# Kernel optimization log

Hardware: AMD Instinct MI355X
Metric: run time of the kernel (lower is better)

## Reference

```python
import jax, jax.numpy as jnp
import numpy as np

N = 100000

def gat_layer(x, src, dst, W, a_s, a_d, b, H, C, concat):
    # x: [N, F_in]; messages flow src -> dst, softmax grouped by dst (PyG GATConv)
    h = (x @ W).reshape(N, H, C)                       # [N,H,C]
    al_s = jnp.sum(h * a_s, axis=-1)                   # [N,H]
    al_d = jnp.sum(h * a_d, axis=-1)                   # [N,H]
    e = jax.nn.leaky_relu(al_s[src] + al_d[dst], 0.2)  # [E,H]
    m = jax.ops.segment_max(e, dst, num_segments=N)    # [N,H] per-dst max
    ex = jnp.exp(e - m[dst])
    s = jax.ops.segment_sum(ex, dst, num_segments=N)
    alpha = ex / (s[dst] + 1e-16)                      # [E,H]
    msg = h[src] * alpha[:, :, None]                   # [E,H,C]
    out = jax.ops.segment_sum(msg, dst, num_segments=N)  # [N,H,C]
    out = out.reshape(N, H * C) if concat else out.mean(axis=1)
    return out + b

def setup_inputs() -> dict:
    key = jax.random.key(0)
    ks = jax.random.split(key, 32)
    d = {}
    d['x'] = jax.random.normal(ks[0], (N, 128), dtype=jnp.float32)
    d['edge_index'] = jax.random.randint(ks[1], (2, 1600000), 0, N, dtype=jnp.int32)
    dims = [(128, 8, 8), (64, 8, 8), (64, 8, 8), (64, 8, 8), (64, 8, 40)]
    for i, (fin, H, C) in enumerate(dims, start=1):
        d[f'W{i}'] = jax.random.normal(ks[4 * i], (fin, H * C), dtype=jnp.float32) * 0.1
        d[f'as{i}'] = jax.random.normal(ks[4 * i + 1], (H, C), dtype=jnp.float32) * 0.1
        d[f'ad{i}'] = jax.random.normal(ks[4 * i + 2], (H, C), dtype=jnp.float32) * 0.1
        d[f'b{i}'] = jnp.zeros((H * C if i < 5 else C,), dtype=jnp.float32)
    return d

def reference(x, edge_index, W1, as1, ad1, b1, W2, as2, ad2, b2, W3, as3, ad3, b3, W4, as4, ad4, b4, W5, as5, ad5, b5):
    # add self-loops (PyG GATConv default add_self_loops=True)
    loop = jnp.arange(N, dtype=edge_index.dtype)
    src = jnp.concatenate([edge_index[0], loop])
    dst = jnp.concatenate([edge_index[1], loop])
    h = gat_layer(x, src, dst, W1, as1, ad1, b1, 8, 8, True)
    h = jax.nn.leaky_relu(h, 0.2)  # dropout is identity in eval mode
    h = gat_layer(h, src, dst, W2, as2, ad2, b2, 8, 8, True)
    h = jax.nn.leaky_relu(h, 0.2)
    h = gat_layer(h, src, dst, W3, as3, ad3, b3, 8, 8, True)
    h = jax.nn.leaky_relu(h, 0.2)
    h = gat_layer(h, src, dst, W4, as4, ad4, b4, 8, 8, True)
    h = jax.nn.leaky_relu(h, 0.2)
    h = gat_layer(h, src, dst, W5, as5, ad5, b5, 8, 40, False)
    return jax.nn.log_softmax(h, axis=1)
```

## Files before the change

kernel.cpp:

```cpp
#include <hip/hip_runtime.h>
#include <cstddef>
#include <cstdint>

static __device__ __forceinline__ float leaky(float x){ return x >= 0.f ? x : 0.2f*x; }
static __device__ __forceinline__ float bfl(unsigned short v){ return __uint_as_float(((unsigned)v)<<16); }
static __device__ __forceinline__ float blo(unsigned u){ return __uint_as_float(u<<16); }
static __device__ __forceinline__ float bhi(unsigned u){ return __uint_as_float(u & 0xffff0000u); }
static __device__ __forceinline__ unsigned bf16r(float f){
  unsigned u = __float_as_uint(f);
  return (u + 0x7fffu + ((u>>16)&1u)) >> 16;
}
static __device__ __forceinline__ unsigned pk(float lo, float hi){
  return bf16r(lo) | (bf16r(hi)<<16);
}

__global__ __launch_bounds__(256) void rs_hist1(const int* __restrict__ edst, int E, int N,
                                                int* __restrict__ hist, int NBLK, int Etot){
  __shared__ int lh[512];
  int t = threadIdx.x, b = blockIdx.x;
  lh[t] = 0; lh[t+256] = 0;
  __syncthreads();
  int base = b*8192;
  for (int i = 0; i < 32; i++){
    int e = base + t + i*256;
    if (e < Etot){
      int d = (e < E) ? edst[e] : (e - E);
      atomicAdd(&lh[d>>8], 1);
    }
  }
  __syncthreads();
  hist[(size_t)t*NBLK + b] = lh[t];
  hist[(size_t)(t+256)*NBLK + b] = lh[t+256];
}
__global__ __launch_bounds__(256) void s_bsum(const int* __restrict__ a, int* __restrict__ bsum, int L){
  __shared__ int sm[256];
  int t = threadIdx.x; int i = blockIdx.x*256 + t;
  sm[t] = (i < L) ? a[i] : 0;
  __syncthreads();
  #pragma unroll
  for (int o=128;o;o>>=1){ if (t<o) sm[t]+=sm[t+o]; __syncthreads(); }
  if (t==0) bsum[blockIdx.x] = sm[0];
}
__global__ __launch_bounds__(512) void k_bscan(const int* __restrict__ bsum, int* __restrict__ boff, int NB){
  __shared__ int sm[512];
  int t = threadIdx.x;
  int v = (t < NB) ? bsum[t] : 0;
  sm[t] = v; __syncthreads();
  for (int o=1;o<512;o<<=1){
    int u = (t>=o) ? sm[t-o] : 0;
    __syncthreads();
    sm[t] += u;
    __syncthreads();
  }
  if (t < NB) boff[t] = sm[t] - v;
  if (t == NB-1) boff[NB] = sm[t];
}
__global__ __launch_bounds__(256) void s_apply(const int* __restrict__ a, const int* __restrict__ boff,
                                               int* __restrict__ out, int L){
  __shared__ int sm[256];
  int t = threadIdx.x, b = blockIdx.x;
  int i = b*256 + t;
  int v = (i < L) ? a[i] : 0;
  sm[t] = v; __syncthreads();
  for (int o=1;o<256;o<<=1){
    int u = (t>=o) ? sm[t-o] : 0;
    __syncthreads();
    sm[t] += u;
    __syncthreads();
  }
  if (i < L) out[i] = boff[b] + sm[t] - v;
}
__global__ __launch_bounds__(256) void rs_scatter1(const int* __restrict__ esrc, const int* __restrict__ edst,
                                                   int E, int N, const int* __restrict__ hist2, int NBLK,
                                                   int* __restrict__ bufA, int Etot){
  __shared__ int gb[512];
  __shared__ int lcnt[512];
  int t = threadIdx.x, b = blockIdx.x;
  gb[t]     = hist2[(size_t)t*NBLK + b];
  gb[t+256] = hist2[(size_t)(t+256)*NBLK + b];
  lcnt[t] = 0; lcnt[t+256] = 0;
  __syncthreads();
  int base = b*8192;
  for (int i = 0; i < 32; i++){
    int e = base + t + i*256;
    if (e < Etot){
      int s, d;
      if (e < E){ s = esrc[e]; d = edst[e]; }
      else { s = e - E; d = s; }
      int bin = d >> 8;
      int r = atomicAdd(&lcnt[bin], 1);
      bufA[gb[bin] + r] = s | ((d & 255) << 17);
    }
  }
}
__global__ __launch_bounds__(256) void rs_lvl2(const int* __restrict__ bufA, const int* __restrict__ hist2,
                                               int NBLK, int* __restrict__ srcs, int* __restrict__ off,
                                               int N, int Etot){
  __shared__ int cnt[256];
  __shared__ int basev[256];
  int t = threadIdx.x, g = blockIdx.x;
  int beg = hist2[(size_t)g*NBLK];
  int end = (g < 511) ? hist2[(size_t)(g+1)*NBLK] : Etot;
  cnt[t] = 0;
  __syncthreads();
  for (int j = beg + t; j < end; j += 256)
    atomicAdd(&cnt[(bufA[j] >> 17) & 255], 1);
  __syncthreads();
  int v = cnt[t];
  for (int o=1;o<256;o<<=1){
    int u = (t>=o) ? cnt[t-o] : 0;
    __syncthreads();
    cnt[t] += u;
    __syncthreads();
  }
  basev[t] = cnt[t] - v;
  __syncthreads();
  cnt[t] = 0;
  __syncthreads();
  for (int j = beg + t; j < end; j += 256){
    int u = bufA[j];
    int lb = (u >> 17) & 255;
    int r = atomicAdd(&cnt[lb], 1);
    srcs[beg + basev[lb] + r] = u & 0x1FFFF;
  }
  int node = g*256 + t;
  if (node < N) off[node] = beg + basev[t];
  if (g == 0 && t == 0) off[N] = Etot;
}

template<int K, int M, bool IB, bool OB, bool AL>
__global__ __launch_bounds__(256) void k_gemm(
    const void* __restrict__ Ain, const float* __restrict__ W, int ldw, int col0,
    void* __restrict__ out, int N,
    const float* __restrict__ a_s, const float* __restrict__ a_d,
    unsigned short* __restrict__ alsO, float* __restrict__ aldO)
{
  constexpr int KT = 64;
  constexpr int TX = M/4;
  __shared__ alignas(16) float As[64][68];
  __shared__ alignas(16) float Ws[KT][M];
  __shared__ float asl[64], adl[64];
  int t = threadIdx.x;
  int base = blockIdx.x*64;
  int tx = t % TX, ty = t / TX;
  bool act = ty < 16;
  int n0 = ty*4, m0 = tx*4;
  if (AL && t < 64){ asl[t] = a_s[t]; adl[t] = a_d[t]; }
  float acc[4][4] = {};
  for (int kt=0; kt<K; kt+=KT){
    if (IB){
      const unsigned short* A16 = (const unsigned short*)Ain;
      for (int i=t; i<64*8; i+=256){
        int n = i >> 3, kq = i & 7;
        uint4 q = make_uint4(0,0,0,0);
        int gn = base + n;
        if (gn < N) q = *(const uint4*)(A16 + (size_t)gn*K + kt + kq*8);
        float* ap = &As[n][kq*8];
        ap[0]=blo(q.x); ap[1]=bhi(q.x); ap[2]=blo(q.y); ap[3]=bhi(q.y);
        ap[4]=blo(q.z); ap[5]=bhi(q.z); ap[6]=blo(q.w); ap[7]=bhi(q.w);
      }
    } else {
      const float* A = (const float*)Ain;
      for (int i=t; i<64*16; i+=256){
        int n  = i >> 4;
        int kq = i & 15;
        float4 v = make_float4(0.f,0.f,0.f,0.f);
        int gn = base + n;
        if (gn < N) v = *(const float4*)(A + (size_t)gn*K + kt + kq*4);
        As[n][kq*4+0]=v.x; As[n][kq*4+1]=v.y; As[n][kq*4+2]=v.z; As[n][kq*4+3]=v.w;
      }
    }
    for (int i=t; i<KT*(M/4); i+=256){
      int k = i/(M/4), mq = i%(M/4);
      *(float4*)&Ws[k][mq*4] = *(const float4*)(W + (size_t)(kt+k)*ldw + col0 + mq*4);
    }
    __syncthreads();
    if (act){
      #pragma unroll 4
      for (int k=0;k<KT;k+=4){
        float4 a0 = *(const float4*)&As[n0+0][k];
        float4 a1 = *(const float4*)&As[n0+1][k];
        float4 a2 = *(const float4*)&As[n0+2][k];
        float4 a3 = *(const float4*)&As[n0+3][k];
        float4 w0 = *(const float4*)&Ws[k+0][m0];
        float4 w1 = *(const float4*)&Ws[k+1][m0];
        float4 w2 = *(const float4*)&Ws[k+2][m0];
        float4 w3 = *(const float4*)&Ws[k+3][m0];
        acc[0][0]=fmaf(a0.x,w0.x,acc[0][0]); acc[0][1]=fmaf(a0.x,w0.y,acc[0][1]);
        acc[0][2]=fmaf(a0.x,w0.z,acc[0][2]); acc[0][3]=fmaf(a0.x,w0.w,acc[0][3]);
        acc[1][0]=fmaf(a1.x,w0.x,acc[1][0]); acc[1][1]=fmaf(a1.x,w0.y,acc[1][1]);
        acc[1][2]=fmaf(a1.x,w0.z,acc[1][2]); acc[1][3]=fmaf(a1.x,w0.w,acc[1][3]);
        acc[2][0]=fmaf(a2.x,w0.x,acc[2][0]); acc[2][1]=fmaf(a2.x,w0.y,acc[2][1]);
        acc[2][2]=fmaf(a2.x,w0.z,acc[2][2]); acc[2][3]=fmaf(a2.x,w0.w,acc[2][3]);
        acc[3][0]=fmaf(a3.x,w0.x,acc[3][0]); acc[3][1]=fmaf(a3.x,w0.y,acc[3][1]);
        acc[3][2]=fmaf(a3.x,w0.z,acc[3][2]); acc[3][3]=fmaf(a3.x,w0.w,acc[3][3]);
        acc[0][0]=fmaf(a0.y,w1.x,acc[0][0]); acc[0][1]=fmaf(a0.y,w1.y,acc[0][1]);
        acc[0][2]=fmaf(a0.y,w1.z,acc[0][2]); acc[0][3]=fmaf(a0.y,w1.w,acc[0][3]);
        acc[1][0]=fmaf(a1.y,w1.x,acc[1][0]); acc[1][1]=fmaf(a1.y,w1.y,acc[1][1]);
        acc[1][2]=fmaf(a1.y,w1.z,acc[1][2]); acc[1][3]=fmaf(a1.y,w1.w,acc[1][3]);
        acc[2][0]=fmaf(a2.y,w1.x,acc[2][0]); acc[2][1]=fmaf(a2.y,w1.y,acc[2][1]);
        acc[2][2]=fmaf(a2.y,w1.z,acc[2][2]); acc[2][3]=fmaf(a2.y,w1.w,acc[2][3]);
        acc[3][0]=fmaf(a3.y,w1.x,acc[3][0]); acc[3][1]=fmaf(a3.y,w1.y,acc[3][1]);
        acc[3][2]=fmaf(a3.y,w1.z,acc[3][2]); acc[3][3]=fmaf(a3.y,w1.w,acc[3][3]);
        acc[0][0]=fmaf(a0.z,w2.x,acc[0][0]); acc[0][1]=fmaf(a0.z,w2.y,acc[0][1]);
        acc[0][2]=fmaf(a0.z,w2.z,acc[0][2]); acc[0][3]=fmaf(a0.z,w2.w,acc[0][3]);
        acc[1][0]=fmaf(a1.z,w2.x,acc[1][0]); acc[1][1]=fmaf(a1.z,w2.y,acc[1][1]);
        acc[1][2]=fmaf(a1.z,w2.z,acc[1][2]); acc[1][3]=fmaf(a1.z,w2.w,acc[1][3]);
        acc[2][0]=fmaf(a2.z,w2.x,acc[2][0]); acc[2][1]=fmaf(a2.z,w2.y,acc[2][1]);
        acc[2][2]=fmaf(a2.z,w2.z,acc[2][2]); acc[2][3]=fmaf(a2.z,w2.w,acc[2][3]);
        acc[3][0]=fmaf(a3.z,w2.x,acc[3][0]); acc[3][1]=fmaf(a3.z,w2.y,acc[3][1]);
        acc[3][2]=fmaf(a3.z,w2.z,acc[3][2]); acc[3][3]=fmaf(a3.z,w2.w,acc[3][3]);
        acc[0][0]=fmaf(a0.w,w3.x,acc[0][0]); acc[0][1]=fmaf(a0.w,w3.y,acc[0][1]);
        acc[0][2]=fmaf(a0.w,w3.z,acc[0][2]); acc[0][3]=fmaf(a0.w,w3.w,acc[0][3]);
        acc[1][0]=fmaf(a1.w,w3.x,acc[1][0]); acc[1][1]=fmaf(a1.w,w3.y,acc[1][1]);
        acc[1][2]=fmaf(a1.w,w3.z,acc[1][2]); acc[1][3]=fmaf(a1.w,w3.w,acc[1][3]);
        acc[2][0]=fmaf(a2.w,w3.x,acc[2][0]); acc[2][1]=fmaf(a2.w,w3.y,acc[2][1]);
        acc[2][2]=fmaf(a2.w,w3.z,acc[2][2]); acc[2][3]=fmaf(a2.w,w3.w,acc[2][3]);
        acc[3][0]=fmaf(a3.w,w3.x,acc[3][0]); acc[3][1]=fmaf(a3.w,w3.y,acc[3][1]);
        acc[3][2]=fmaf(a3.w,w3.z,acc[3][2]); acc[3][3]=fmaf(a3.w,w3.w,acc[3][3]);
      }
    }
    __syncthreads();
  }
  if (act){
    #pragma unroll
    for (int i=0;i<4;i++){
      int gn = base + n0 + i;
      if (gn < N){
        if (OB){
          unsigned p0 = pk(acc[i][0], acc[i][1]);
          unsigned p1 = pk(acc[i][2], acc[i][3]);
          *(uint2*)((unsigned short*)out + (size_t)gn*M + m0) = make_uint2(p0, p1);
        } else {
          float4 v = make_float4(acc[i][0],acc[i][1],acc[i][2],acc[i][3]);
          *(float4*)((float*)out + (size_t)gn*M + m0) = v;
        }
      }
    }
    if (AL){
      int hd2 = tx >> 1;
      int c0  = hd2*8 + (tx & 1)*4;
      float w0s=asl[c0], w1s=asl[c0+1], w2s=asl[c0+2], w3s=asl[c0+3];
      float w0d=adl[c0], w1d=adl[c0+1], w2d=adl[c0+2], w3d=adl[c0+3];
      #pragma unroll
      for (int i=0;i<4;i++){
        int gn = base + n0 + i;
        float ps = acc[i][0]*w0s + acc[i][1]*w1s + acc[i][2]*w2s + acc[i][3]*w3s;
        float pd = acc[i][0]*w0d + acc[i][1]*w1d + acc[i][2]*w2d + acc[i][3]*w3d;
        ps += __shfl_xor(ps, 1, 64);
        pd += __shfl_xor(pd, 1, 64);
        if (((tx & 1) == 0) && gn < N){
          alsO[(size_t)gn*8 + hd2] = (unsigned short)bf16r(ps);
          aldO[(size_t)gn*8 + hd2] = pd;
        }
      }
    }
  }
}

__global__ __launch_bounds__(320) void k_gemm5(
    const unsigned short* __restrict__ z16, const float* __restrict__ Wf,
    float* __restrict__ out5, int base, int cnt)
{
  __shared__ float As[64][65];
  __shared__ alignas(16) float Ws[64][40];
  int t = threadIdx.x;
  int rb = blockIdx.x*64;
  int tx = t % 10, ty = t / 10;
  int n0 = ty*2, m0 = tx*4;
  float acc[2][4] = {};
  for (int kt = 0; kt < 512; kt += 64){
    for (int i = t; i < 512; i += 320){
      int n = i >> 3, kq = i & 7;
      uint4 q = make_uint4(0,0,0,0);
      int ln = rb + n;
      if (ln < cnt) q = *(const uint4*)(z16 + (size_t)ln*512 + kt + kq*8);
      float* ap = &As[n][kq*8];
      ap[0]=blo(q.x); ap[1]=bhi(q.x); ap[2]=blo(q.y); ap[3]=bhi(q.y);
      ap[4]=blo(q.z); ap[5]=bhi(q.z); ap[6]=blo(q.w); ap[7]=bhi(q.w);
    }
    for (int i = t; i < 640; i += 320){
      int k = i / 10, mq = i % 10;
      *(float4*)&Ws[k][mq*4] = *(const float4*)(Wf + (size_t)(kt+k)*40 + mq*4);
    }
    __syncthreads();
    #pragma unroll 8
    for (int k=0;k<64;k++){
      float4 w = *(const float4*)&Ws[k][m0];
      float a0 = As[n0][k], a1 = As[n0+1][k];
      acc[0][0]=fmaf(a0,w.x,acc[0][0]); acc[0][1]=fmaf(a0,w.y,acc[0][1]);
      acc[0][2]=fmaf(a0,w.z,acc[0][2]); acc[0][3]=fmaf(a0,w.w,acc[0][3]);
      acc[1][0]=fmaf(a1,w.x,acc[1][0]); acc[1][1]=fmaf(a1,w.y,acc[1][1]);
      acc[1][2]=fmaf(a1,w.z,acc[1][2]); acc[1][3]=fmaf(a1,w.w,acc[1][3]);
    }
    __syncthreads();
  }
  #pragma unroll
  for (int r=0;r<2;r++){
    int ln = rb + n0 + r;
    if (ln < cnt){
      *(float4*)(out5 + (size_t)(base+ln)*40 + m0) =
        make_float4(acc[r][0],acc[r][1],acc[r][2],acc[r][3]);
    }
  }
}

template<bool FOLD5>
__global__ __launch_bounds__(256) void k_agg64(
    const unsigned short* __restrict__ h16, const unsigned short* __restrict__ al16,
    const float* __restrict__ al_d, const int* __restrict__ off,
    const int* __restrict__ srcs, const float* __restrict__ bias,
    unsigned short* __restrict__ outf, int N, int apply_act,
    const float* __restrict__ wsb, const float* __restrict__ wdb,
    unsigned short* __restrict__ als5, float* __restrict__ ald5)
{
  int t = threadIdx.x;
  int grp = t >> 3;
  int sub = t & 7;
  int node = blockIdx.x*32 + grp;
  if (node >= N) return;
  int beg = off[node], end = off[node+1];
  float ald = al_d[(size_t)node*8 + sub];
  float s = 0.f;
  float acc[8] = {0.f,0.f,0.f,0.f,0.f,0.f,0.f,0.f};
  int j = beg;
  for (; j+3 < end; j += 4){
    int s0 = srcs[j], s1 = srcs[j+1], s2 = srcs[j+2], s3 = srcs[j+3];
    float e0 = leaky(bfl(al16[(size_t)s0*8 + sub]) + ald);
    float e1 = leaky(bfl(al16[(size_t)s1*8 + sub]) + ald);
    float e2 = leaky(bfl(al16[(size_t)s2*8 + sub]) + ald);
    float e3 = leaky(bfl(al16[(size_t)s3*8 + sub]) + ald);
    float a0 = __expf(e0), a1 = __expf(e1), a2 = __expf(e2), a3 = __expf(e3);
    uint4 q0 = *(const uint4*)(h16 + (size_t)s0*64 + sub*8);
    uint4 q1 = *(const uint4*)(h16 + (size_t)s1*64 + sub*8);
    uint4 q2 = *(const uint4*)(h16 + (size_t)s2*64 + sub*8);
    uint4 q3 = *(const uint4*)(h16 + (size_t)s3*64 + sub*8);
    s += a0 + a1 + a2 + a3;
    acc[0]=fmaf(a0,blo(q0.x),acc[0]); acc[1]=fmaf(a0,bhi(q0.x),acc[1]);
    acc[2]=fmaf(a0,blo(q0.y),acc[2]); acc[3]=fmaf(a0,bhi(q0.y),acc[3]);
    acc[4]=fmaf(a0,blo(q0.z),acc[4]); acc[5]=fmaf(a0,bhi(q0.z),acc[5]);
    acc[6]=fmaf(a0,blo(q0.w),acc[6]); acc[7]=fmaf(a0,bhi(q0.w),acc[7]);
    acc[0]=fmaf(a1,blo(q1.x),acc[0]); acc[1]=fmaf(a1,bhi(q1.x),acc[1]);
    acc[2]=fmaf(a1,blo(q1.y),acc[2]); acc[3]=fmaf(a1,bhi(q1.y),acc[3]);
    acc[4]=fmaf(a1,blo(q1.z),acc[4]); acc[5]=fmaf(a1,bhi(q1.z),acc[5]);
    acc[6]=fmaf(a1,blo(q1.w),acc[6]); acc[7]=fmaf(a1,bhi(q1.w),acc[7]);
    acc[0]=fmaf(a2,blo(q2.x),acc[0]); acc[1]=fmaf(a2,bhi(q2.x),acc[1]);
    acc[2]=fmaf(a2,blo(q2.y),acc[2]); acc[3]=fmaf(a2,bhi(q2.y),acc[3]);
    acc[4]=fmaf(a2,blo(q2.z),acc[4]); acc[5]=fmaf(a2,bhi(q2.z),acc[5]);
    acc[6]=fmaf(a2,blo(q2.w),acc[6]); acc[7]=fmaf(a2,bhi(q2.w),acc[7]);
    acc[0]=fmaf(a3,blo(q3.x),acc[0]); acc[1]=fmaf(a3,bhi(q3.x),acc[1]);
    acc[2]=fmaf(a3,blo(q3.y),acc[2]); acc[3]=fmaf(a3,bhi(q3.y),acc[3]);
    acc[4]=fmaf(a3,blo(q3.z),acc[4]); acc[5]=fmaf(a3,bhi(q3.z),acc[5]);
    acc[6]=fmaf(a3,blo(q3.w),acc[6]); acc[7]=fmaf(a3,bhi(q3.w),acc[7]);
  }
  for (; j < end; ++j){
    int s0 = srcs[j];
    float a = __expf(leaky(bfl(al16[(size_t)s0*8 + sub]) + ald));
    uint4 q0 = *(const uint4*)(h16 + (size_t)s0*64 + sub*8);
    s += a;
    acc[0]=fmaf(a,blo(q0.x),acc[0]); acc[1]=fmaf(a,bhi(q0.x),acc[1]);
    acc[2]=fmaf(a,blo(q0.y),acc[2]); acc[3]=fmaf(a,bhi(q0.y),acc[3]);
    acc[4]=fmaf(a,blo(q0.z),acc[4]); acc[5]=fmaf(a,bhi(q0.z),acc[5]);
    acc[6]=fmaf(a,blo(q0.w),acc[6]); acc[7]=fmaf(a,bhi(q0.w),acc[7]);
  }
  float inv = 1.f/(s + 1e-16f);
  const float4* bp = (const float4*)(bias + sub*8);
  float4 b0 = bp[0], b1 = bp[1];
  float r0 = acc[0]*inv + b0.x, r1 = acc[1]*inv + b0.y;
  float r2 = acc[2]*inv + b0.z, r3 = acc[3]*inv + b0.w;
  float r4 = acc[4]*inv + b1.x, r5 = acc[5]*inv + b1.y;
  float r6 = acc[6]*inv + b1.z, r7 = acc[7]*inv + b1.w;
  if (apply_act){
    r0=leaky(r0); r1=leaky(r1); r2=leaky(r2); r3=leaky(r3);
    r4=leaky(r4); r5=leaky(r5); r6=leaky(r6); r7=leaky(r7);
  }
  uint4 o;
  o.x = pk(r0,r1); o.y = pk(r2,r3); o.z = pk(r4,r5); o.w = pk(r6,r7);
  *(uint4*)(outf + (size_t)node*64 + sub*8) = o;
  if (FOLD5){
    float ps[8], pd[8];
    #pragma unroll
    for (int h=0;h<8;h++){
      const float4* wsp = (const float4*)(wsb + h*64 + sub*8);
      float4 u0 = wsp[0], u1 = wsp[1];
      ps[h] = r0*u0.x + r1*u0.y + r2*u0.z + r3*u0.w
            + r4*u1.x + r5*u1.y + r6*u1.z + r7*u1.w;
      const float4* wdp = (const float4*)(wdb + h*64 + sub*8);
      float4 v0 = wdp[0], v1 = wdp[1];
      pd[h] = r0*v0.x + r1*v0.y + r2*v0.z + r3*v0.w
            + r4*v1.x + r5*v1.y + r6*v1.z + r7*v1.w;
    }
    #pragma unroll
    for (int m=1;m<8;m<<=1){
      #pragma unroll
      for (int h=0;h<8;h++){
        ps[h] += __shfl_xor(ps[h], m, 64);
        pd[h] += __shfl_xor(pd[h], m, 64);
      }
    }
    float vs = ps[0], vd = pd[0];
    #pragma unroll
    for (int h=1;h<8;h++){ if (sub == h){ vs = ps[h]; vd = pd[h]; } }
    als5[(size_t)node*8 + sub] = (unsigned short)bf16r(vs);
    ald5[(size_t)node*8 + sub] = vd;
  }
}

__global__ __launch_bounds__(512) void k_ws(const float* __restrict__ W5,
                                            const float* __restrict__ as5,
                                            const float* __restrict__ ad5,
                                            float* __restrict__ ws, float* __restrict__ wd){
  int t = threadIdx.x;
  int h = t >> 6, k = t & 63;
  float s = 0.f, d = 0.f;
  #pragma unroll 8
  for (int c=0;c<40;c++){
    float w = W5[(size_t)k*320 + h*40 + c];
    s = fmaf(w, as5[h*40+c], s);
    d = fmaf(w, ad5[h*40+c], d);
  }
  ws[h*64+k] = s; wd[h*64+k] = d;
}
__global__ void k_wf(const float* __restrict__ W5, float* __restrict__ Wf){
  int i = blockIdx.x*256 + threadIdx.x;
  if (i >= 512*40) return;
  int row = i / 40, c = i - row*40;
  int h = row >> 6, k = row & 63;
  Wf[i] = W5[(size_t)k*320 + h*40 + c];
}

__global__ __launch_bounds__(256) void k_agg5z(
    const unsigned short* __restrict__ f16, const unsigned short* __restrict__ al16,
    const float* __restrict__ al_d, const int* __restrict__ off,
    const int* __restrict__ srcs, unsigned short* __restrict__ z16, int base, int cnt)
{
  int t = threadIdx.x;
  int w = t >> 6;
  int ln = blockIdx.x*4 + w;
  if (ln >= cnt) return;
  int node = base + ln;
  int tl = t & 63;
  int hd = tl & 7;
  int cb = tl >> 3;
  int beg = off[node], end = off[node+1];
  float ald = al_d[(size_t)node*8 + hd];
  int lanebase = hd*4;
  int cbo = cb*8;
  float s = 0.f;
  float acc[8] = {0.f,0.f,0.f,0.f,0.f,0.f,0.f,0.f};
  int jb = beg;
  float atil = 0.f; int si = 0;
  {
    int j = jb + cb;
    if (j < end){ si = srcs[j]; atil = __expf(leaky(bfl(al16[(size_t)si*8 + hd]) + ald)); }
  }
  while (jb < end){
    int jb2 = jb + 8;
    float atil2 = 0.f; int si2 = 0;
    {
      int j2 = jb2 + cb;
      if (j2 < end){ si2 = srcs[j2]; atil2 = __expf(leaky(bfl(al16[(size_t)si2*8 + hd]) + ald)); }
    }
    s += atil;
    int nfull = end - jb; if (nfull > 8) nfull = 8;
    #pragma unroll 8
    for (int e = 0; e < 8; e++){
      if (e >= nfull) break;
      float ae = __uint_as_float(__builtin_amdgcn_ds_bpermute(lanebase + e*32, __float_as_uint(atil)));
      int sie = __builtin_amdgcn_readlane(si, e*8);
      uint4 q = *(const uint4*)(f16 + (size_t)sie*64 + cbo);
      acc[0]=fmaf(ae,blo(q.x),acc[0]); acc[1]=fmaf(ae,bhi(q.x),acc[1]);
      acc[2]=fmaf(ae,blo(q.y),acc[2]); acc[3]=fmaf(ae,bhi(q.y),acc[3]);
      acc[4]=fmaf(ae,blo(q.z),acc[4]); acc[5]=fmaf(ae,bhi(q.z),acc[5]);
      acc[6]=fmaf(ae,blo(q.w),acc[6]); acc[7]=fmaf(ae,bhi(q.w),acc[7]);
    }
    atil = atil2; si = si2; jb = jb2;
  }
  s += __shfl_xor(s, 8, 64);
  s += __shfl_xor(s, 16, 64);
  s += __shfl_xor(s, 32, 64);
  float inv = 1.f/(s + 1e-16f);
  uint4 o;
  o.x = pk(acc[0]*inv, acc[1]*inv);
  o.y = pk(acc[2]*inv, acc[3]*inv);
  o.z = pk(acc[4]*inv, acc[5]*inv);
  o.w = pk(acc[6]*inv, acc[7]*inv);
  *(uint4*)(z16 + (size_t)ln*512 + hd*64 + cbo) = o;
}

__global__ __launch_bounds__(256) void k_final(
    const float* __restrict__ acc, const float* __restrict__ b5,
    float* __restrict__ out, int N)
{
  int t = threadIdx.x;
  int node = blockIdx.x*4 + (t >> 6);
  if (node >= N) return;
  int tl = t & 63;
  float v = (tl < 40) ? acc[(size_t)node*40 + tl]*0.125f + b5[tl] : -1e30f;
  float m = v;
  #pragma unroll
  for (int o=32;o;o>>=1) m = fmaxf(m, __shfl_xor(m, o, 64));
  float ex = (tl < 40) ? __expf(v - m) : 0.f;
  float s = ex;
  #pragma unroll
  for (int o=32;o;o>>=1) s += __shfl_xor(s, o, 64);
  if (tl < 40) out[(size_t)node*40 + tl] = (v - m) - __logf(s);
}

extern "C" void kernel_launch(void* const* d_in, const int* in_sizes, int n_in,
                              void* d_out, int out_size, void* d_ws, size_t ws_size,
                              hipStream_t stream) {
  const float* x  = (const float*)d_in[0];
  const int*   ei = (const int*)d_in[1];
  const int N = in_sizes[0] / 128;
  const int E = in_sizes[1] / 2;
  const int* esrc = ei;
  const int* edst = ei + E;
  const float* W1 = (const float*)d_in[2];
  const float* as1= (const float*)d_in[3];
  const float* ad1= (const float*)d_in[4];
  const float* b1 = (const float*)d_in[5];
  const float* W2 = (const float*)d_in[6];
  const float* as2= (const float*)d_in[7];
  const float* ad2= (const float*)d_in[8];
  const float* b2 = (const float*)d_in[9];
  const float* W3 = (const float*)d_in[10];
  const float* as3= (const float*)d_in[11];
  const float* ad3= (const float*)d_in[12];
  const float* b3 = (const float*)d_in[13];
  const float* W4 = (const float*)d_in[14];
  const float* as4= (const float*)d_in[15];
  const float* ad4= (const float*)d_in[16];
  const float* b4 = (const float*)d_in[17];
  const float* W5 = (const float*)d_in[18];
  const float* as5= (const float*)d_in[19];
  const float* ad5= (const float*)d_in[20];
  const float* b5 = (const float*)d_in[21];

  char* p = (char*)d_ws;
  auto alloc = [&](size_t bytes)->void*{
    uintptr_t u = (uintptr_t)p;
    u = (u + 255) & ~(uintptr_t)255;
    void* r = (void*)u;
    p = (char*)u + bytes;
    return r;
  };
  const int Etot = E + N;
  const int NBLK = (Etot + 8191)/8192;
  const int L    = 512*NBLK;
  const int NB2  = (L + 255)/256;
  const int NG   = (N + 255)/256;

  int* off    = (int*)alloc((size_t)(N+1)*4);
  int* srcs   = (int*)alloc((size_t)Etot*4);
  int* hist   = (int*)alloc((size_t)L*4);
  int* hist2  = (int*)alloc((size_t)L*4);
  int* hb     = (int*)alloc((size_t)(NB2+1)*4);
  unsigned short* al_s16 = (unsigned short*)alloc((size_t)N*8*2);
  float* al_d = (float*)alloc((size_t)N*8*4);
  unsigned short* al5s16 = (unsigned short*)alloc((size_t)N*8*2);
  float* al5d = (float*)alloc((size_t)N*8*4);
  unsigned short* h16  = (unsigned short*)alloc((size_t)N*64*2);
  unsigned short* fA16 = (unsigned short*)alloc((size_t)N*64*2);
  unsigned short* fB16 = (unsigned short*)alloc((size_t)N*64*2);
  float* wsb  = (float*)alloc((size_t)8*64*4);
  float* wdb  = (float*)alloc((size_t)8*64*4);
  float* Wf   = (float*)alloc((size_t)512*40*4);
  float* out5 = (float*)alloc((size_t)N*40*4);
  unsigned short* zbuf = h16;
  int* bufA   = (int*)h16;

  int gT = (N+63)/64, gA = (N+3)/4;
  int gA64 = (N+31)/32;

  rs_hist1  <<<NBLK,256,0,stream>>>(edst, E, N, hist, NBLK, Etot);
  s_bsum    <<<NB2,256,0,stream>>>(hist, hb, L);
  k_bscan   <<<1,512,0,stream>>>(hb, hb, NB2);
  s_apply   <<<NB2,256,0,stream>>>(hist, hb, hist2, L);
  rs_scatter1<<<NBLK,256,0,stream>>>(esrc, edst, E, N, hist2, NBLK, bufA, Etot);
  rs_lvl2   <<<NG,256,0,stream>>>(bufA, hist2, NBLK, srcs, off, N, Etot);

  k_ws<<<1,512,0,stream>>>(W5, as5, ad5, wsb, wdb);
  k_wf<<<(512*40+255)/256,256,0,stream>>>(W5, Wf);

  k_gemm<128,64,false,true,true><<<gT,256,0,stream>>>(x, W1, 64, 0, h16, N, as1, ad1, al_s16, al_d);
  k_agg64<false><<<gA64,256,0,stream>>>(h16, al_s16, al_d, off, srcs, b1, fA16, N, 1,
                                        nullptr, nullptr, nullptr, nullptr);

  k_gemm<64,64,true,true,true><<<gT,256,0,stream>>>(fA16, W2, 64, 0, h16, N, as2, ad2, al_s16, al_d);
  k_agg64<false><<<gA64,256,0,stream>>>(h16, al_s16, al_d, off, srcs, b2, fB16, N, 1,
                                        nullptr, nullptr, nullptr, nullptr);

  k_gemm<64,64,true,true,true><<<gT,256,0,stream>>>(fB16, W3, 64, 0, h16, N, as3, ad3, al_s16, al_d);
  k_agg64<false><<<gA64,256,0,stream>>>(h16, al_s16, al_d, off, srcs, b3, fA16, N, 1,
                                        nullptr, nullptr, nullptr, nullptr);

  k_gemm<64,64,true,true,true><<<gT,256,0,stream>>>(fA16, W4, 64, 0, h16, N, as4, ad4, al_s16, al_d);
  k_agg64<true><<<gA64,256,0,stream>>>(h16, al_s16, al_d, off, srcs, b4, fB16, N, 1,
                                       wsb, wdb, al5s16, al5d);

  const int CH = 25000;
  for (int base = 0; base < N; base += CH){
    int cnt = (N - base < CH) ? (N - base) : CH;
    k_agg5z<<<(cnt+3)/4,256,0,stream>>>(fB16, al5s16, al5d, off, srcs, zbuf, base, cnt);
    k_gemm5<<<(cnt+63)/64,320,0,stream>>>(zbuf, Wf, out5, base, cnt);
  }

  k_final<<<gA,256,0,stream>>>(out5, b5, (float*)d_out, N);
}
```

Measured before the change: 657.1 us.

## Fuse final bias+log_softmax into gemm5 epilogue and split shared histogram counters

Folds the mean-over-heads scale, bias and log_softmax into the k_gemm5 epilogue, staging results through shared memory, and drops the separate k_final kernel and the out5 buffer. This removes one launch plus a full N×40 float write and re-read. It also duplicates the shared-memory histogram bins in rs_hist1 and rs_lvl2 by odd/even thread to cut LDS atomic contention. The epilogue runs serially over 40 columns in 64 threads, and its row-wise global writes are uncoalesced.

```diff
diff --git a/kernel.cpp b/kernel.cpp
--- a/kernel.cpp
+++ b/kernel.cpp
@@ -16,21 +16,22 @@
 
 __global__ __launch_bounds__(256) void rs_hist1(const int* __restrict__ edst, int E, int N,
                                                 int* __restrict__ hist, int NBLK, int Etot){
-  __shared__ int lh[512];
+  __shared__ int lh[1024];
   int t = threadIdx.x, b = blockIdx.x;
-  lh[t] = 0; lh[t+256] = 0;
+  lh[t] = 0; lh[t+256] = 0; lh[t+512] = 0; lh[t+768] = 0;
   __syncthreads();
   int base = b*8192;
+  int sub = (t & 1) << 9;
   for (int i = 0; i < 32; i++){
     int e = base + t + i*256;
     if (e < Etot){
       int d = (e < E) ? edst[e] : (e - E);
-      atomicAdd(&lh[d>>8], 1);
-    }
-  }
-  __syncthreads();
-  hist[(size_t)t*NBLK + b] = lh[t];
-  hist[(size_t)(t+256)*NBLK + b] = lh[t+256];
+      atomicAdd(&lh[sub | (d>>8)], 1);
+    }
+  }
+  __syncthreads();
+  hist[(size_t)t*NBLK + b] = lh[t] + lh[t+512];
+  hist[(size_t)(t+256)*NBLK + b] = lh[t+256] + lh[t+768];
 }
 __global__ __launch_bounds__(256) void s_bsum(const int* __restrict__ a, int* __restrict__ bsum, int L){
   __shared__ int sm[256];
@@ -97,14 +98,18 @@
                                                int NBLK, int* __restrict__ srcs, int* __restrict__ off,
                                                int N, int Etot){
   __shared__ int cnt[256];
+  __shared__ int cnt2[512];
   __shared__ int basev[256];
   int t = threadIdx.x, g = blockIdx.x;
   int beg = hist2[(size_t)g*NBLK];
   int end = (g < 511) ? hist2[(size_t)(g+1)*NBLK] : Etot;
-  cnt[t] = 0;
-  __syncthreads();
+  cnt2[t] = 0; cnt2[t+256] = 0;
+  __syncthreads();
+  int sub = (t & 1) << 8;
   for (int j = beg + t; j < end; j += 256)
-    atomicAdd(&cnt[(bufA[j] >> 17) & 255], 1);
+    atomicAdd(&cnt2[sub | ((bufA[j] >> 17) & 255)], 1);
+  __syncthreads();
+  cnt[t] = cnt2[t] + cnt2[t+256];
   __syncthreads();
   int v = cnt[t];
   for (int o=1;o<256;o<<=1){
@@ -260,7 +265,7 @@
 
 __global__ __launch_bounds__(320) void k_gemm5(
     const unsigned short* __restrict__ z16, const float* __restrict__ Wf,
-    float* __restrict__ out5, int base, int cnt)
+    const float* __restrict__ b5, float* __restrict__ outp, int base, int cnt)
 {
   __shared__ float As[64][65];
   __shared__ alignas(16) float Ws[64][40];
@@ -297,10 +302,25 @@
   }
   #pragma unroll
   for (int r=0;r<2;r++){
-    int ln = rb + n0 + r;
+    As[n0+r][m0+0] = acc[r][0]*0.125f + b5[m0+0];
+    As[n0+r][m0+1] = acc[r][1]*0.125f + b5[m0+1];
+    As[n0+r][m0+2] = acc[r][2]*0.125f + b5[m0+2];
+    As[n0+r][m0+3] = acc[r][3]*0.125f + b5[m0+3];
+  }
+  __syncthreads();
+  if (t < 64){
+    int ln = rb + t;
     if (ln < cnt){
-      *(float4*)(out5 + (size_t)(base+ln)*40 + m0) =
-        make_float4(acc[r][0],acc[r][1],acc[r][2],acc[r][3]);
+      float m = -1e30f;
+      #pragma unroll 8
+      for (int c=0;c<40;c++) m = fmaxf(m, As[t][c]);
+      float s = 0.f;
+      #pragma unroll 8
+      for (int c=0;c<40;c++) s += __expf(As[t][c] - m);
+      float lg = m + __logf(s);
+      float* op = outp + (size_t)(base+ln)*40;
+      #pragma unroll 8
+      for (int c=0;c<40;c++) op[c] = As[t][c] - lg;
     }
   }
 }
@@ -488,25 +508,6 @@
   *(uint4*)(z16 + (size_t)ln*512 + hd*64 + cbo) = o;
 }
 
-__global__ __launch_bounds__(256) void k_final(
-    const float* __restrict__ acc, const float* __restrict__ b5,
-    float* __restrict__ out, int N)
-{
-  int t = threadIdx.x;
-  int node = blockIdx.x*4 + (t >> 6);
-  if (node >= N) return;
-  int tl = t & 63;
-  float v = (tl < 40) ? acc[(size_t)node*40 + tl]*0.125f + b5[tl] : -1e30f;
-  float m = v;
-  #pragma unroll
-  for (int o=32;o;o>>=1) m = fmaxf(m, __shfl_xor(m, o, 64));
-  float ex = (tl < 40) ? __expf(v - m) : 0.f;
-  float s = ex;
-  #pragma unroll
-  for (int o=32;o;o>>=1) s += __shfl_xor(s, o, 64);
-  if (tl < 40) out[(size_t)node*40 + tl] = (v - m) - __logf(s);
-}
-
 extern "C" void kernel_launch(void* const* d_in, const int* in_sizes, int n_in,
                               void* d_out, int out_size, void* d_ws, size_t ws_size,
                               hipStream_t stream) {
@@ -566,11 +567,10 @@
   float* wsb  = (float*)alloc((size_t)8*64*4);
   float* wdb  = (float*)alloc((size_t)8*64*4);
   float* Wf   = (float*)alloc((size_t)512*40*4);
-  float* out5 = (float*)alloc((size_t)N*40*4);
   unsigned short* zbuf = h16;
   int* bufA   = (int*)h16;
 
-  int gT = (N+63)/64, gA = (N+3)/4;
+  int gT = (N+63)/64;
   int gA64 = (N+31)/32;
 
   rs_hist1  <<<NBLK,256,0,stream>>>(edst, E, N, hist, NBLK, Etot);
@@ -603,8 +603,6 @@
   for (int base = 0; base < N; base += CH){
     int cnt = (N - base < CH) ? (N - base) : CH;
     k_agg5z<<<(cnt+3)/4,256,0,stream>>>(fB16, al5s16, al5d, off, srcs, zbuf, base, cnt);
-    k_gemm5<<<(cnt+63)/64,320,0,stream>>>(zbuf, Wf, out5, base, cnt);
-  }
-
-  k_final<<<gA,256,0,stream>>>(out5, b5, (float*)d_out, N);
-}
+    k_gemm5<<<(cnt+63)/64,320,0,stream>>>(zbuf, Wf, b5, (float*)d_out, base, cnt);
+  }
+}
```

After: 648.7 us (median of 2 runs). No clear change (-1.3%).
